# Kernel optimization log

Hardware: AMD Instinct MI355X
Metric: run time of the kernel (lower is better)

## Reference

```python
import jax, jax.numpy as jnp
import numpy as np

H = 8          # num_heads
MAXP = 64      # max_temporal_length
EPS = 1e-5

def setup_inputs() -> dict:
    key = jax.random.key(0)
    ks = jax.random.split(key, 8)
    b, c, t, h, w = 2, 512, 16, 32, 32
    s = 0.02
    return {
        "x": jax.random.normal(ks[0], (b, c, t, h, w), jnp.float32),
        "ln_g": jnp.ones((c,), jnp.float32),
        "ln_b": jnp.zeros((c,), jnp.float32),
        "qkv_w": jax.random.normal(ks[1], (3 * c, c), jnp.float32) * s,
        "qkv_b": jax.random.normal(ks[2], (3 * c,), jnp.float32) * s,
        "k_table": jax.random.normal(ks[3], (2 * MAXP + 1, c // H), jnp.float32) * s,
        "v_table": jax.random.normal(ks[4], (2 * MAXP + 1, c // H), jnp.float32) * s,
        "proj_w": jax.random.normal(ks[5], (c, c), jnp.float32) * s,
        "proj_b": jax.random.normal(ks[6], (c,), jnp.float32) * s,
    }

def reference(x, ln_g, ln_b, qkv_w, qkv_b, k_table, v_table, proj_w, proj_b):
    b, c, t, h, w = x.shape
    ch = c // H
    B = b * h * w
    # (b c t h w) -> (b*h*w, t, c)
    seq = jnp.transpose(x, (0, 3, 4, 2, 1)).reshape(B, t, c)
    # LayerNorm
    mu = seq.mean(-1, keepdims=True)
    var = seq.var(-1, keepdims=True)
    nrm = (seq - mu) * jax.lax.rsqrt(var + EPS) * ln_g + ln_b
    # QKV projection: (B, t, 3c)
    qkv = nrm @ qkv_w.T + qkv_b
    q, k, v = jnp.split(qkv, 3, axis=-1)            # each (B, t, c)
    q = q.reshape(B, t, H, ch)
    k = k.reshape(B, t, H, ch)
    v = v.reshape(B, t, H, ch)
    # relative position lookup: (t, t, ch)
    idx = jnp.clip(jnp.arange(t)[None, :] - jnp.arange(t)[:, None], -MAXP, MAXP) + MAXP
    k_rp = k_table[idx]
    v_rp = v_table[idx]
    scale = 1.0 / math_sqrt_sqrt(ch)
    qs = q * scale
    # scores: content + relative-position key term
    weight = jnp.einsum('bqhc,bkhc->bhqk', qs, k * scale)
    weight = weight + jnp.einsum('bqhc,qkc->bhqk', qs, k_rp * scale)
    attn = jax.nn.softmax(weight, axis=-1)
    # values: content + relative-position value term
    a = jnp.einsum('bhqk,bkhc->bqhc', attn, v)
    a = a + jnp.einsum('bhqk,qkc->bqhc', attn, v_rp)
    a = a.reshape(B, t, c)
    out = a @ proj_w.T + proj_b                      # (B, t, c)
    out = out.reshape(b, h, w, t, c).transpose(0, 4, 3, 1, 2)
    return x + out

def math_sqrt_sqrt(ch):
    return float(np.sqrt(np.sqrt(ch)))
```

## Files before the change

### kernel.cpp

```cpp
#include <hip/hip_runtime.h>
#include <cstdint>
#include <cstddef>

#define Cc   512
#define Tt   16
#define HWn  1024
#define NBat 2
#define Mtot (NBat*Tt*HWn)
#define Hh   8
#define CHd  64
#define NQKV 1536

typedef _Float16 half8 __attribute__((ext_vector_type(8)));
typedef float    f32x4 __attribute__((ext_vector_type(4)));

__device__ __forceinline__ void gl_lds16(const void* g, void* l) {
  __builtin_amdgcn_global_load_lds(
      (const __attribute__((address_space(1))) unsigned int*)g,
      (__attribute__((address_space(3))) unsigned int*)l, 16, 0, 0);
}

__global__ __launch_bounds__(256) void wconv_k(const float* __restrict__ qw,
                                               const float* __restrict__ pw,
                                               _Float16* __restrict__ wq,
                                               _Float16* __restrict__ wp) {
  int i = blockIdx.x * 256 + threadIdx.x;
  if (i < NQKV * Cc) wq[i] = (_Float16)qw[i];
  if (i < Cc * Cc)   wp[i] = (_Float16)pw[i];
}

__global__ __launch_bounds__(256) void ln_k(const float* __restrict__ x,
                                            const float* __restrict__ g,
                                            const float* __restrict__ bln,
                                            _Float16* __restrict__ Ah) {
  int blk = blockIdx.x;
  int bi = blk >> 6, ti = (blk >> 2) & 15, hwc = blk & 3;
  int t = threadIdx.x;
  int hw = hwc * 256 + t;
  const float* xp = x + ((size_t)bi * Cc * Tt + ti) * HWn + hw;
  float s = 0.f, s2 = 0.f;
  #pragma unroll 8
  for (int ci = 0; ci < Cc; ++ci) {
    float v = xp[(size_t)ci * (Tt * HWn)];
    s += v; s2 += v * v;
  }
  float mean = s * (1.f / Cc);
  float var  = s2 * (1.f / Cc) - mean * mean;
  float rs   = rsqrtf(var + 1e-5f);
  size_t m = ((size_t)(bi * Tt + ti)) * HWn + hw;
  _Float16* dst = Ah + m * Cc;
  for (int k0 = 0; k0 < Cc; k0 += 8) {
    half8 hv;
    #pragma unroll
    for (int u = 0; u < 8; ++u) {
      int ci = k0 + u;
      float v = xp[(size_t)ci * (Tt * HWn)];
      hv[u] = (_Float16)((v - mean) * rs * g[ci] + bln[ci]);
    }
    *(half8*)(dst + k0) = hv;
  }
}

template<int NCOLS, bool PROJ>
__global__ __launch_bounds__(256) void gemm_k(const _Float16* __restrict__ A,
                                              const _Float16* __restrict__ W,
                                              const float* __restrict__ bias,
                                              _Float16* __restrict__ Cout,
                                              const float* __restrict__ xres,
                                              float* __restrict__ outF) {
  __shared__ union {
    struct { _Float16 A[3][128 * 32]; _Float16 B[3][128 * 32]; } s;
    float Cs[64 * 129];
  } u;

  const int tid  = threadIdx.x;
  const int wave = tid >> 6, lane = tid & 63;
  const int NTN = NCOLS / 128;
  const int tile_m = blockIdx.x / NTN;
  const int tile_n = blockIdx.x % NTN;
  const int m0 = tile_m * 128, n0 = tile_n * 128;
  const int wm = wave >> 1, wn = wave & 1;
  const int fr = lane & 15;
  const int fkc = lane >> 4;
  const int fsw = (fr >> 1) & 3;

  f32x4 acc[4][4] = {};

  const int srow_l = lane >> 2;
  const int schunk = lane & 3;

  auto stage = [&](int buf, int kt) {
    const int k0 = kt * 32;
    #pragma unroll
    for (int i = 0; i < 2; ++i) {
      int rowbase = i * 64 + wave * 16;
      int row = rowbase + srow_l;
      int cg = schunk ^ ((row >> 1) & 3);
      const _Float16* sa = A + (size_t)(m0 + row) * Cc + k0 + cg * 8;
      gl_lds16(sa, &u.s.A[buf][rowbase * 32]);
      const _Float16* sb = W + (size_t)(n0 + row) * Cc + k0 + cg * 8;
      gl_lds16(sb, &u.s.B[buf][rowbase * 32]);
    }
  };

  const int NK = Cc / 32;
  stage(0, 0);
  stage(1, 1);
  asm volatile("s_waitcnt vmcnt(4)" ::: "memory");
  __builtin_amdgcn_s_barrier();

  int bc = 0, b1 = 1, b2 = 2;
  for (int kt = 0; kt < NK; ++kt) {
    if (kt + 2 < NK) stage(b2, kt + 2);
    half8 af[4], bf[4];
    #pragma unroll
    for (int i = 0; i < 4; ++i) {
      int row = wm * 64 + i * 16 + fr;
      af[i] = *(const half8*)&u.s.A[bc][row * 32 + ((fkc ^ fsw) * 8)];
    }
    #pragma unroll
    for (int j = 0; j < 4; ++j) {
      int row = wn * 64 + j * 16 + fr;
      bf[j] = *(const half8*)&u.s.B[bc][row * 32 + ((fkc ^ fsw) * 8)];
    }
    #pragma unroll
    for (int i = 0; i < 4; ++i)
      #pragma unroll
      for (int j = 0; j < 4; ++j)
        acc[i][j] = __builtin_amdgcn_mfma_f32_16x16x32_f16(af[i], bf[j], acc[i][j], 0, 0, 0);
    if (kt < NK - 1) {
      if (kt + 2 < NK) asm volatile("s_waitcnt vmcnt(4)" ::: "memory");
      else             asm volatile("s_waitcnt vmcnt(0)" ::: "memory");
      __builtin_amdgcn_s_barrier();
    }
    int t0 = bc; bc = b1; b1 = b2; b2 = t0;
  }
  __syncthreads();

  const int bi_o = m0 >> 14, ti_o = (m0 >> 10) & 15, hw0 = m0 & 1023;
  #pragma unroll
  for (int r = 0; r < 2; ++r) {
    if (wm == r) {
      #pragma unroll
      for (int i = 0; i < 4; ++i)
        #pragma unroll
        for (int j = 0; j < 4; ++j)
          #pragma unroll
          for (int jj = 0; jj < 4; ++jj) {
            int row = i * 16 + (lane >> 4) * 4 + jj;
            int col = wn * 64 + j * 16 + (lane & 15);
            u.Cs[row * 129 + col] = acc[i][j][jj];
          }
    }
    __syncthreads();
    if (!PROJ) {
      for (int it = 0; it < 32; ++it) {
        int row = it * 2 + (tid >> 7);
        int col = tid & 127;
        float v = u.Cs[row * 129 + col] + bias[n0 + col];
        Cout[(size_t)(m0 + r * 64 + row) * NCOLS + n0 + col] = (_Float16)v;
      }
    } else {
      for (int it = 0; it < 32; ++it) {
        int col = it * 4 + (tid >> 6);
        int row = tid & 63;
        size_t oidx = (((size_t)(bi_o * Cc + n0 + col) * Tt) + ti_o) * HWn
                      + hw0 + r * 64 + row;
        outF[oidx] = u.Cs[row * 129 + col] + bias[n0 + col] + xres[oidx];
      }
    }
    __syncthreads();
  }
}

__global__ __launch_bounds__(256) void attn_k(const _Float16* __restrict__ qkv,
                                              const float* __restrict__ ktab,
                                              const float* __restrict__ vtab,
                                              _Float16* __restrict__ aout) {
  __shared__ float kt_s[31][64], vt_s[31][64];
  int bx = blockIdx.x;
  int bi = bx >> 9, h = (bx >> 6) & 7, hwc = bx & 63;
  int t = threadIdx.x;
  int qi = t >> 4, hwl = t & 15;
  int hw = hwc * 16 + hwl;

  for (int i = t; i < 31 * 64; i += 256) {
    (&kt_s[0][0])[i] = ktab[49 * 64 + i];
    (&vt_s[0][0])[i] = vtab[49 * 64 + i];
  }
  __syncthreads();

  size_t mq = ((size_t)(bi * Tt + qi)) * HWn + hw;
  const _Float16* qrow = qkv + mq * NQKV + h * CHd;
  float q[64];
  #pragma unroll
  for (int u = 0; u < 8; ++u) {
    half8 hv = *(const half8*)(qrow + u * 8);
    #pragma unroll
    for (int c = 0; c < 8; ++c) q[u * 8 + c] = (float)hv[c];
  }

  float s[16];
  #pragma unroll
  for (int ki = 0; ki < 16; ++ki) {
    size_t mk = ((size_t)(bi * Tt + ki)) * HWn + hw;
    const _Float16* krow = qkv + mk * NQKV + Cc + h * CHd;
    int d = ki - qi + 15;
    float acc = 0.f;
    #pragma unroll
    for (int u = 0; u < 8; ++u) {
      half8 hv = *(const half8*)(krow + u * 8);
      #pragma unroll
      for (int c = 0; c < 8; ++c)
        acc += q[u * 8 + c] * ((float)hv[c] + kt_s[d][u * 8 + c]);
    }
    s[ki] = acc * 0.125f;
  }

  float mx = s[0];
  #pragma unroll
  for (int ki = 1; ki < 16; ++ki) mx = fmaxf(mx, s[ki]);
  float sum = 0.f;
  #pragma unroll
  for (int ki = 0; ki < 16; ++ki) { s[ki] = __expf(s[ki] - mx); sum += s[ki]; }
  float inv = 1.f / sum;

  float o[64];
  #pragma unroll
  for (int c = 0; c < 64; ++c) o[c] = 0.f;
  #pragma unroll
  for (int ki = 0; ki < 16; ++ki) {
    size_t mk = ((size_t)(bi * Tt + ki)) * HWn + hw;
    const _Float16* vrow = qkv + mk * NQKV + 2 * Cc + h * CHd;
    int d = ki - qi + 15;
    float pk = s[ki];
    #pragma unroll
    for (int u = 0; u < 8; ++u) {
      half8 hv = *(const half8*)(vrow + u * 8);
      #pragma unroll
      for (int c = 0; c < 8; ++c)
        o[u * 8 + c] += pk * ((float)hv[c] + vt_s[d][u * 8 + c]);
    }
  }

  _Float16* arow = aout + mq * Cc + h * CHd;
  #pragma unroll
  for (int u = 0; u < 8; ++u) {
    half8 hv;
    #pragma unroll
    for (int c = 0; c < 8; ++c) hv[c] = (_Float16)(o[u * 8 + c] * inv);
    *(half8*)(arow + u * 8) = hv;
  }
}

extern "C" void kernel_launch(void* const* d_in, const int* in_sizes, int n_in,
                              void* d_out, int out_size, void* d_ws, size_t ws_size,
                              hipStream_t stream) {
  const float* x      = (const float*)d_in[0];
  const float* ln_g   = (const float*)d_in[1];
  const float* ln_b   = (const float*)d_in[2];
  const float* qkv_w  = (const float*)d_in[3];
  const float* qkv_b  = (const float*)d_in[4];
  const float* k_tab  = (const float*)d_in[5];
  const float* v_tab  = (const float*)d_in[6];
  const float* proj_w = (const float*)d_in[7];
  const float* proj_b = (const float*)d_in[8];
  float* out = (float*)d_out;

  _Float16* Ah   = (_Float16*)d_ws;
  _Float16* qkvb = Ah   + (size_t)Mtot * Cc;
  _Float16* ab   = qkvb + (size_t)Mtot * NQKV;
  _Float16* wq   = ab   + (size_t)Mtot * Cc;
  _Float16* wp   = wq   + (size_t)NQKV * Cc;

  wconv_k<<<3072, 256, 0, stream>>>(qkv_w, proj_w, wq, wp);
  ln_k<<<128, 256, 0, stream>>>(x, ln_g, ln_b, Ah);
  gemm_k<NQKV, false><<<(Mtot / 128) * (NQKV / 128), 256, 0, stream>>>(
      Ah, wq, qkv_b, qkvb, nullptr, nullptr);
  attn_k<<<1024, 256, 0, stream>>>(qkvb, k_tab, v_tab, ab);
  gemm_k<Cc, true><<<(Mtot / 128) * (Cc / 128), 256, 0, stream>>>(
      ab, wp, proj_b, nullptr, x, out);
}
```

Measured before the change: 496.0 us.

## Use packed fp16 math and register prefetch in the temporal attention kernel

```diff
diff --git a/kernel.cpp b/kernel.cpp
--- a/kernel.cpp
+++ b/kernel.cpp
@@ -11,13 +11,22 @@
 #define CHd  64
 #define NQKV 1536
 
-typedef _Float16 half8 __attribute__((ext_vector_type(8)));
-typedef float    f32x4 __attribute__((ext_vector_type(4)));
+typedef _Float16 half8  __attribute__((ext_vector_type(8)));
+typedef _Float16 half2t __attribute__((ext_vector_type(2)));
+typedef float    f32x4  __attribute__((ext_vector_type(4)));
 
 __device__ __forceinline__ void gl_lds16(const void* g, void* l) {
   __builtin_amdgcn_global_load_lds(
       (const __attribute__((address_space(1))) unsigned int*)g,
       (__attribute__((address_space(3))) unsigned int*)l, 16, 0, 0);
+}
+
+__device__ __forceinline__ float fdot2h(half2t a, half2t b, float c) {
+#if __has_builtin(__builtin_amdgcn_fdot2)
+  return __builtin_amdgcn_fdot2(a, b, c, false);
+#else
+  return c + (float)a[0] * (float)b[0] + (float)a[1] * (float)b[1];
+#endif
 }
 
 __global__ __launch_bounds__(256) void wconv_k(const float* __restrict__ qw,
@@ -177,7 +186,8 @@
                                               const float* __restrict__ ktab,
                                               const float* __restrict__ vtab,
                                               _Float16* __restrict__ aout) {
-  __shared__ float kt_s[31][64], vt_s[31][64];
+  __shared__ alignas(16) _Float16 kt_s[31 * 72];
+  __shared__ alignas(16) _Float16 vt_s[31 * 72];
   int bx = blockIdx.x;
   int bi = bx >> 9, h = (bx >> 6) & 7, hwc = bx & 63;
   int t = threadIdx.x;
@@ -185,36 +195,54 @@
   int hw = hwc * 16 + hwl;
 
   for (int i = t; i < 31 * 64; i += 256) {
-    (&kt_s[0][0])[i] = ktab[49 * 64 + i];
-    (&vt_s[0][0])[i] = vtab[49 * 64 + i];
+    int r = i >> 6, c = i & 63;
+    kt_s[r * 72 + c] = (_Float16)ktab[(49 + r) * 64 + c];
+    vt_s[r * 72 + c] = (_Float16)vtab[(49 + r) * 64 + c];
   }
   __syncthreads();
 
   size_t mq = ((size_t)(bi * Tt + qi)) * HWn + hw;
-  const _Float16* qrow = qkv + mq * NQKV + h * CHd;
-  float q[64];
-  #pragma unroll
-  for (int u = 0; u < 8; ++u) {
-    half8 hv = *(const half8*)(qrow + u * 8);
-    #pragma unroll
-    for (int c = 0; c < 8; ++c) q[u * 8 + c] = (float)hv[c];
+  size_t m0 = ((size_t)(bi * Tt + 0)) * HWn + hw;
+  const size_t kstride = (size_t)HWn * NQKV;
+
+  half8 qh[8];
+  {
+    const _Float16* qrow = qkv + mq * NQKV + h * CHd;
+    #pragma unroll
+    for (int u = 0; u < 8; ++u) qh[u] = ((const half8*)qrow)[u];
   }
 
   float s[16];
-  #pragma unroll
-  for (int ki = 0; ki < 16; ++ki) {
-    size_t mk = ((size_t)(bi * Tt + ki)) * HWn + hw;
-    const _Float16* krow = qkv + mk * NQKV + Cc + h * CHd;
-    int d = ki - qi + 15;
-    float acc = 0.f;
-    #pragma unroll
-    for (int u = 0; u < 8; ++u) {
-      half8 hv = *(const half8*)(krow + u * 8);
-      #pragma unroll
-      for (int c = 0; c < 8; ++c)
-        acc += q[u * 8 + c] * ((float)hv[c] + kt_s[d][u * 8 + c]);
-    }
-    s[ki] = acc * 0.125f;
+  {
+    const _Float16* kp = qkv + m0 * NQKV + Cc + h * CHd;
+    half8 kr[8], nx[8];
+    #pragma unroll
+    for (int u = 0; u < 8; ++u) kr[u] = ((const half8*)kp)[u];
+    for (int ki = 0; ki < 16; ++ki) {
+      const _Float16* knext = kp + kstride;
+      if (ki < 15) {
+        #pragma unroll
+        for (int u = 0; u < 8; ++u) nx[u] = ((const half8*)knext)[u];
+      }
+      int d = ki - qi + 15;
+      const _Float16* tp = &kt_s[d * 72];
+      float a0 = 0.f, a1 = 0.f, a2 = 0.f, a3 = 0.f;
+      #pragma unroll
+      for (int u = 0; u < 8; ++u) {
+        half8 tv = *(const half8*)(tp + u * 8);
+        half8 sm = kr[u] + tv;
+        const half2t* s2 = (const half2t*)&sm;
+        const half2t* q2 = (const half2t*)&qh[u];
+        a0 = fdot2h(q2[0], s2[0], a0);
+        a1 = fdot2h(q2[1], s2[1], a1);
+        a2 = fdot2h(q2[2], s2[2], a2);
+        a3 = fdot2h(q2[3], s2[3], a3);
+      }
+      s[ki] = ((a0 + a1) + (a2 + a3)) * 0.125f;
+      #pragma unroll
+      for (int u = 0; u < 8; ++u) kr[u] = nx[u];
+      kp = knext;
+    }
   }
 
   float mx = s[0];
@@ -225,21 +253,35 @@
   for (int ki = 0; ki < 16; ++ki) { s[ki] = __expf(s[ki] - mx); sum += s[ki]; }
   float inv = 1.f / sum;
 
-  float o[64];
-  #pragma unroll
-  for (int c = 0; c < 64; ++c) o[c] = 0.f;
-  #pragma unroll
-  for (int ki = 0; ki < 16; ++ki) {
-    size_t mk = ((size_t)(bi * Tt + ki)) * HWn + hw;
-    const _Float16* vrow = qkv + mk * NQKV + 2 * Cc + h * CHd;
-    int d = ki - qi + 15;
-    float pk = s[ki];
-    #pragma unroll
-    for (int u = 0; u < 8; ++u) {
-      half8 hv = *(const half8*)(vrow + u * 8);
-      #pragma unroll
-      for (int c = 0; c < 8; ++c)
-        o[u * 8 + c] += pk * ((float)hv[c] + vt_s[d][u * 8 + c]);
+  half8 o8[8];
+  #pragma unroll
+  for (int u = 0; u < 8; ++u) o8[u] = (half8)(_Float16)0.0f;
+  {
+    const _Float16* vp = qkv + m0 * NQKV + 2 * Cc + h * CHd;
+    half8 vr[8], nx[8];
+    #pragma unroll
+    for (int u = 0; u < 8; ++u) vr[u] = ((const half8*)vp)[u];
+    for (int ki = 0; ki < 16; ++ki) {
+      const _Float16* vnext = vp + kstride;
+      if (ki < 15) {
+        #pragma unroll
+        for (int u = 0; u < 8; ++u) nx[u] = ((const half8*)vnext)[u];
+      }
+      int d = ki - qi + 15;
+      const _Float16* tp = &vt_s[d * 72];
+      _Float16 ph = (_Float16)s[ki];
+      half8 pk8;
+      #pragma unroll
+      for (int j = 0; j < 8; ++j) pk8[j] = ph;
+      #pragma unroll
+      for (int u = 0; u < 8; ++u) {
+        half8 tv = *(const half8*)(tp + u * 8);
+        half8 sm = vr[u] + tv;
+        o8[u] += pk8 * sm;
+      }
+      #pragma unroll
+      for (int u = 0; u < 8; ++u) vr[u] = nx[u];
+      vp = vnext;
     }
   }
 
@@ -248,7 +290,7 @@
   for (int u = 0; u < 8; ++u) {
     half8 hv;
     #pragma unroll
-    for (int c = 0; c < 8; ++c) hv[c] = (_Float16)(o[u * 8 + c] * inv);
+    for (int c = 0; c < 8; ++c) hv[c] = (_Float16)((float)o8[u][c] * inv);
     *(half8*)(arow + u * 8) = hv;
   }
 }
```

Measured after the change: 497.4 us. Within noise of the previous version (+0.3%).
